# Kernel optimization log

Hardware: AMD Instinct MI355X
Metric: run time of the kernel (lower is better)

Reference implementation:

```python
import jax, jax.numpy as jnp
import numpy as np

D_MODEL = 1024
N_HEAD = 16
AGENT_NUM = 256


def setup_inputs() -> dict:
    key = jax.random.key(0)
    ks = jax.random.split(key, 11)
    B, S, D = 4, 2048, D_MODEL
    s = 1.0 / np.sqrt(D)
    return {
        "q": jax.random.normal(ks[0], (B, S, D), jnp.float32),
        "k": jax.random.normal(ks[1], (B, S, D), jnp.float32),
        "v": jax.random.normal(ks[2], (B, S, D), jnp.float32),
        "Wq": jax.random.normal(ks[3], (D, D), jnp.float32) * s,
        "bq": jnp.zeros((D,), jnp.float32),
        "Wk": jax.random.normal(ks[4], (D, D), jnp.float32) * s,
        "bk": jnp.zeros((D,), jnp.float32),
        "Wv": jax.random.normal(ks[5], (D, D), jnp.float32) * s,
        "bv": jnp.zeros((D,), jnp.float32),
        "Wo": jax.random.normal(ks[6], (D, D), jnp.float32) * s,
        "bo": jnp.zeros((D,), jnp.float32),
    }


def _split_heads(x, n_head):
    B, S, D = x.shape
    return x.reshape(B, S, n_head, D // n_head).transpose(0, 2, 1, 3)  # [B,H,S,d]


def reference(q, k, v, Wq, bq, Wk, bk, Wv, bv, Wo, bo):
    B, S, D = q.shape
    H, A = N_HEAD, AGENT_NUM
    d = D // H
    scale = 1.0 / jnp.sqrt(jnp.asarray(d, q.dtype))

    # QKV linear projections (torch Linear: x @ W.T + b)
    qh = _split_heads(q @ Wq.T + bq, H)  # [B,H,S,d]
    kh = _split_heads(k @ Wk.T + bk, H)
    vh = _split_heads(v @ Wv.T + bv, H)

    # Agent tokens: average-pool queries along sequence down to A tokens
    agent = qh.reshape(B, H, A, S // A, d).mean(axis=3)  # [B,H,A,d]

    # Stage 1: agents aggregate from keys/values (softmax over S)
    agent_attn = jax.nn.softmax(
        jnp.einsum("bhad,bhsd->bhas", agent, kh) * scale, axis=-1)  # [B,H,A,S]
    agent_v = jnp.einsum("bhas,bhsd->bhad", agent_attn, vh)  # [B,H,A,d]

    # Stage 2: queries attend to agent tokens (softmax over A)
    q_attn = jax.nn.softmax(
        jnp.einsum("bhsd,bhad->bhsa", qh, agent) * scale, axis=-1)  # [B,H,S,A]
    out_h = jnp.einsum("bhsa,bhad->bhsd", q_attn, agent_v)  # [B,H,S,d]

    # concat heads + output projection
    out = out_h.transpose(0, 2, 1, 3).reshape(B, S, D)
    out = out @ Wo.T + bo
    return out, q_attn
```

## Files before the change

kernel.cpp:

```cpp
#include <hip/hip_runtime.h>

constexpr int Bsz = 4, Ssz = 2048, Dsz = 1024, Hn = 16, dh = 64, An = 256;

typedef __attribute__((ext_vector_type(8))) short bf16x8;
typedef __attribute__((ext_vector_type(4))) float f32x4;

__device__ __forceinline__ unsigned short f2bf_rn(float f) {
    unsigned int u = __float_as_uint(f);
    return (unsigned short)((u + 0x7FFFu + ((u >> 16) & 1u)) >> 16);
}
__device__ __forceinline__ float bf2f(unsigned short h) {
    return __uint_as_float(((unsigned int)h) << 16);
}
__device__ __forceinline__ void bf_split(float f, unsigned short& hi, unsigned short& lo) {
    hi = f2bf_rn(f);
    lo = f2bf_rn(f - bf2f(hi));
}
__device__ __forceinline__ void gload16(const unsigned short* g, unsigned short* l) {
    __builtin_amdgcn_global_load_lds(
        (const __attribute__((address_space(1))) unsigned int*)g,
        (__attribute__((address_space(3))) unsigned int*)l, 16, 0, 0);
}

template<int LOGC, int NISS>
__device__ __forceinline__ void stage_tile(const unsigned short* __restrict__ g, long rowStride,
                                           unsigned short* lbase, int t) {
    const int wid = t >> 6;
    #pragma unroll
    for (int i = 0; i < NISS; ++i) {
        int slot = i * 256 + t;
        int r = slot >> LOGC;
        int c = slot & ((1 << LOGC) - 1);
        int cs = (c ^ (r & 7)) & ((1 << LOGC) - 1);
        gload16(g + (long)r * rowStride + cs * 8, lbase + (i * 256 + wid * 64) * 8);
    }
}

template<int ROWLEN>
__device__ __forceinline__ bf16x8 fragR(const unsigned short* buf, int row, int ks, int lane) {
    int c = ks * 4 + (lane >> 4);
    int cs = (c ^ (row & 7)) & (ROWLEN / 8 - 1);
    return *reinterpret_cast<const bf16x8*>(buf + row * ROWLEN + cs * 8);
}

__global__ __launch_bounds__(256)
void split_kernel(const float* __restrict__ x, unsigned short* __restrict__ hi,
                  unsigned short* __restrict__ lo, int n4)
{
    int i = blockIdx.x * 256 + threadIdx.x;
    if (i >= n4) return;
    float4 v = reinterpret_cast<const float4*>(x)[i];
    ushort4 h, l;
    bf_split(v.x, h.x, l.x);
    bf_split(v.y, h.y, l.y);
    bf_split(v.z, h.z, l.z);
    bf_split(v.w, h.w, l.w);
    reinterpret_cast<ushort4*>(hi)[i] = h;
    reinterpret_cast<ushort4*>(lo)[i] = l;
}

#define MT 128
#define BKm 32

__device__ __forceinline__ bf16x8 lds_frag(const unsigned short* buf, int baseRow, int lane) {
    int row = baseRow + (lane & 15);
    int c = lane >> 4;
    int idx = row * 32 + ((c ^ ((row >> 1) & 3)) << 3);
    return *reinterpret_cast<const bf16x8*>(buf + idx);
}

template<int OMODE>
__global__ __launch_bounds__(256, 2)
void gemm_nt_mfma3(const unsigned short* __restrict__ Ahi, const unsigned short* __restrict__ Alo,
                   const unsigned short* __restrict__ Bhi, const unsigned short* __restrict__ Blo,
                   const float* __restrict__ bias, float* __restrict__ Cf,
                   unsigned short* __restrict__ Chi, unsigned short* __restrict__ Clo,
                   int K, int N)
{
    __shared__ unsigned short lds[4 * 4096];
    const int t = threadIdx.x;
    const int lane = t & 63, wid = t >> 6;
    const int wr = wid >> 1, wc = wid & 1;
    const int m0 = blockIdx.y * MT, n0 = blockIdx.x * MT;

    const int srow0 = t >> 2;
    const int x4 = t & 3;
    const int ldsBase0 = (wid * 64) * 8;
    const int ldsBase1 = (256 + wid * 64) * 8;

    f32x4 acc[4][4];
    #pragma unroll
    for (int i = 0; i < 4; ++i)
        #pragma unroll
        for (int j = 0; j < 4; ++j)
            acc[i][j] = f32x4{0.f, 0.f, 0.f, 0.f};

    const unsigned short* gA[2] = {Ahi, Alo};
    const unsigned short* gB[2] = {Bhi, Blo};

    for (int k0 = 0; k0 < K; k0 += BKm) {
        #pragma unroll
        for (int hb = 0; hb < 2; ++hb) {
            {
                const unsigned short* G = gA[hb];
                int r0 = srow0, r1 = srow0 + 64;
                int c0 = x4 ^ ((r0 >> 1) & 3);
                int c1 = x4 ^ ((r1 >> 1) & 3);
                gload16(G + (size_t)(m0 + r0) * K + k0 + c0 * 8, lds + hb * 4096 + ldsBase0);
                gload16(G + (size_t)(m0 + r1) * K + k0 + c1 * 8, lds + hb * 4096 + ldsBase1);
            }
            {
                const unsigned short* G = gB[hb];
                int r0 = srow0, r1 = srow0 + 64;
                int c0 = x4 ^ ((r0 >> 1) & 3);
                int c1 = x4 ^ ((r1 >> 1) & 3);
                gload16(G + (size_t)(n0 + r0) * K + k0 + c0 * 8, lds + (2 + hb) * 4096 + ldsBase0);
                gload16(G + (size_t)(n0 + r1) * K + k0 + c1 * 8, lds + (2 + hb) * 4096 + ldsBase1);
            }
        }
        __syncthreads();

        bf16x8 ah[4], al[4], bh[4], bl[4];
        #pragma unroll
        for (int mi = 0; mi < 4; ++mi) {
            ah[mi] = lds_frag(lds + 0 * 4096, wr * 64 + mi * 16, lane);
            al[mi] = lds_frag(lds + 1 * 4096, wr * 64 + mi * 16, lane);
        }
        #pragma unroll
        for (int ni = 0; ni < 4; ++ni) {
            bh[ni] = lds_frag(lds + 2 * 4096, wc * 64 + ni * 16, lane);
            bl[ni] = lds_frag(lds + 3 * 4096, wc * 64 + ni * 16, lane);
        }
        #pragma unroll
        for (int mi = 0; mi < 4; ++mi)
            #pragma unroll
            for (int ni = 0; ni < 4; ++ni) {
                acc[mi][ni] = __builtin_amdgcn_mfma_f32_16x16x32_bf16(ah[mi], bh[ni], acc[mi][ni], 0, 0, 0);
                acc[mi][ni] = __builtin_amdgcn_mfma_f32_16x16x32_bf16(ah[mi], bl[ni], acc[mi][ni], 0, 0, 0);
                acc[mi][ni] = __builtin_amdgcn_mfma_f32_16x16x32_bf16(al[mi], bh[ni], acc[mi][ni], 0, 0, 0);
            }
        __syncthreads();
    }

    #pragma unroll
    for (int mi = 0; mi < 4; ++mi) {
        #pragma unroll
        for (int ni = 0; ni < 4; ++ni) {
            const int n = n0 + wc * 64 + ni * 16 + (lane & 15);
            const float bval = bias[n];
            #pragma unroll
            for (int j = 0; j < 4; ++j) {
                const int m = m0 + wr * 64 + mi * 16 + ((lane >> 4) << 2) + j;
                float val = acc[mi][ni][j] + bval;
                if constexpr (OMODE == 0) {
                    Cf[(size_t)m * N + n] = val;
                } else {
                    const int b = m >> 11, s = m & (Ssz - 1);
                    const int h = n >> 6, c = n & (dh - 1);
                    size_t idx;
                    if constexpr (OMODE == 1)
                        idx = (((size_t)(b * Hn + h)) * Ssz + s) * dh + c;
                    else
                        idx = (((size_t)(b * Hn + h)) * dh + c) * Ssz + s;
                    unsigned short hi, lo;
                    bf_split(val, hi, lo);
                    Chi[idx] = hi; Clo[idx] = lo;
                }
            }
        }
    }
}

__global__ __launch_bounds__(256)
void pool_agent(const unsigned short* __restrict__ qh_hi, const unsigned short* __restrict__ qh_lo,
                unsigned short* __restrict__ ag_hi, unsigned short* __restrict__ ag_lo)
{
    const int idx = blockIdx.x * 256 + threadIdx.x;
    const int c = idx & (dh - 1);
    const int a = (idx >> 6) & (An - 1);
    const int bh = idx >> 14;
    const size_t base = ((size_t)bh * Ssz + a * 8) * dh + c;
    float s = 0.f;
    #pragma unroll
    for (int j = 0; j < 8; ++j)
        s += bf2f(qh_hi[base + j * dh]) + bf2f(qh_lo[base + j * dh]);
    s *= 0.125f;
    unsigned short hi, lo;
    bf_split(s, hi, lo);
    ag_hi[idx] = hi; ag_lo[idx] = lo;
}

__global__ __launch_bounds__(256, 2)
void flash1(const unsigned short* __restrict__ ag_hi, const unsigned short* __restrict__ ag_lo,
            const unsigned short* __restrict__ kh_hi, const unsigned short* __restrict__ kh_lo,
            const unsigned short* __restrict__ vt_hi_g, const unsigned short* __restrict__ vt_lo_g,
            unsigned short* __restrict__ avt_hi, unsigned short* __restrict__ avt_lo)
{
    __shared__ unsigned short lds[32768];
    unsigned short* agh = lds;
    unsigned short* agl = lds + 4096;
    unsigned short* kth = lds + 8192;
    unsigned short* ktl = lds + 12288;
    unsigned short* vth = lds + 16384;
    unsigned short* vtl = lds + 20480;
    const int t = threadIdx.x;
    const int lane = t & 63, w = t >> 6;
    unsigned short* pwh = lds + 24576 + w * 2048;
    unsigned short* pwl = pwh + 1024;

    const int bh = blockIdx.y;
    const int a0 = blockIdx.x * 64;

    stage_tile<3, 2>(ag_hi + ((size_t)bh * An + a0) * dh, dh, agh, t);
    stage_tile<3, 2>(ag_lo + ((size_t)bh * An + a0) * dh, dh, agl, t);

    f32x4 O[4];
    #pragma unroll
    for (int i = 0; i < 4; ++i) O[i] = f32x4{0.f, 0.f, 0.f, 0.f};
    float m_run = -INFINITY, l_run = 0.f;

    bf16x8 bqh[2], bql[2];
    bool haveQ = false;

    for (int s0 = 0; s0 < Ssz; s0 += 64) {
        stage_tile<3, 2>(kh_hi + ((size_t)bh * Ssz + s0) * dh, dh, kth, t);
        stage_tile<3, 2>(kh_lo + ((size_t)bh * Ssz + s0) * dh, dh, ktl, t);
        stage_tile<3, 2>(vt_hi_g + (size_t)bh * dh * Ssz + s0, Ssz, vth, t);
        stage_tile<3, 2>(vt_lo_g + (size_t)bh * dh * Ssz + s0, Ssz, vtl, t);
        __syncthreads();

        if (!haveQ) {
            #pragma unroll
            for (int ks = 0; ks < 2; ++ks) {
                bqh[ks] = fragR<64>(agh, w * 16 + (lane & 15), ks, lane);
                bql[ks] = fragR<64>(agl, w * 16 + (lane & 15), ks, lane);
            }
            haveQ = true;
        }

        f32x4 sc[4];
        #pragma unroll
        for (int si = 0; si < 4; ++si) sc[si] = f32x4{0.f, 0.f, 0.f, 0.f};
        #pragma unroll
        for (int si = 0; si < 4; ++si)
            #pragma unroll
            for (int ks = 0; ks < 2; ++ks) {
                bf16x8 ah = fragR<64>(kth, si * 16 + (lane & 15), ks, lane);
                bf16x8 al = fragR<64>(ktl, si * 16 + (lane & 15), ks, lane);
                sc[si] = __builtin_amdgcn_mfma_f32_16x16x32_bf16(ah, bqh[ks], sc[si], 0, 0, 0);
                sc[si] = __builtin_amdgcn_mfma_f32_16x16x32_bf16(ah, bql[ks], sc[si], 0, 0, 0);
                sc[si] = __builtin_amdgcn_mfma_f32_16x16x32_bf16(al, bqh[ks], sc[si], 0, 0, 0);
            }

        float tmax = -INFINITY;
        #pragma unroll
        for (int si = 0; si < 4; ++si)
            #pragma unroll
            for (int j = 0; j < 4; ++j) {
                sc[si][j] *= 0.125f;
                tmax = fmaxf(tmax, sc[si][j]);
            }
        tmax = fmaxf(tmax, __shfl_xor(tmax, 16));
        tmax = fmaxf(tmax, __shfl_xor(tmax, 32));
        float newm = fmaxf(m_run, tmax);
        float fac = __expf(m_run - newm);
        float tsum = 0.f;
        #pragma unroll
        for (int si = 0; si < 4; ++si)
            #pragma unroll
            for (int j = 0; j < 4; ++j) {
                float p = __expf(sc[si][j] - newm);
                sc[si][j] = p;
                tsum += p;
            }
        tsum += __shfl_xor(tsum, 16);
        tsum += __shfl_xor(tsum, 32);
        l_run = l_run * fac + tsum;
        m_run = newm;

        const int aloc = lane & 15;
        #pragma unroll
        for (int si = 0; si < 4; ++si) {
            ushort4 h4, l4;
            bf_split(sc[si][0], h4.x, l4.x);
            bf_split(sc[si][1], h4.y, l4.y);
            bf_split(sc[si][2], h4.z, l4.z);
            bf_split(sc[si][3], h4.w, l4.w);
            int baseS = si * 16 + ((lane >> 4) << 2);
            int addr = aloc * 64 + (baseS ^ ((aloc & 7) << 3));
            *reinterpret_cast<ushort4*>(pwh + addr) = h4;
            *reinterpret_cast<ushort4*>(pwl + addr) = l4;
        }

        float fj[4];
        #pragma unroll
        for (int j = 0; j < 4; ++j) fj[j] = __shfl(fac, ((lane >> 4) << 2) + j);
        #pragma unroll
        for (int di = 0; di < 4; ++di)
            #pragma unroll
            for (int j = 0; j < 4; ++j) O[di][j] *= fj[j];

        #pragma unroll
        for (int ks = 0; ks < 2; ++ks) {
            bf16x8 pah = fragR<64>(pwh, lane & 15, ks, lane);
            bf16x8 pal = fragR<64>(pwl, lane & 15, ks, lane);
            #pragma unroll
            for (int di = 0; di < 4; ++di) {
                bf16x8 vh = fragR<64>(vth, di * 16 + (lane & 15), ks, lane);
                bf16x8 vl = fragR<64>(vtl, di * 16 + (lane & 15), ks, lane);
                O[di] = __builtin_amdgcn_mfma_f32_16x16x32_bf16(pah, vh, O[di], 0, 0, 0);
                O[di] = __builtin_amdgcn_mfma_f32_16x16x32_bf16(pah, vl, O[di], 0, 0, 0);
                O[di] = __builtin_amdgcn_mfma_f32_16x16x32_bf16(pal, vh, O[di], 0, 0, 0);
            }
        }
        __syncthreads();
    }

    float lj[4];
    #pragma unroll
    for (int j = 0; j < 4; ++j) lj[j] = __shfl(l_run, ((lane >> 4) << 2) + j);
    #pragma unroll
    for (int di = 0; di < 4; ++di)
        #pragma unroll
        for (int j = 0; j < 4; ++j) {
            float val = O[di][j] / lj[j];
            int d = di * 16 + (lane & 15);
            int aG = a0 + w * 16 + ((lane >> 4) << 2) + j;
            size_t idx = ((size_t)bh * dh + d) * An + aG;
            unsigned short hi, lo;
            bf_split(val, hi, lo);
            avt_hi[idx] = hi; avt_lo[idx] = lo;
        }
}

__global__ __launch_bounds__(256, 1)
void flash2(const unsigned short* __restrict__ qh_hi, const unsigned short* __restrict__ qh_lo,
            const unsigned short* __restrict__ ag_hi, const unsigned short* __restrict__ ag_lo,
            const unsigned short* __restrict__ avt_hi, const unsigned short* __restrict__ avt_lo,
            float* __restrict__ q_attn,
            unsigned short* __restrict__ xo_hi, unsigned short* __restrict__ xo_lo)
{
    __shared__ unsigned short lds[65536];
    unsigned short* agh = lds;
    unsigned short* agl = lds + 16384;
    unsigned short* qhh = lds + 32768;
    unsigned short* qhl = lds + 36864;

    const int t = threadIdx.x;
    const int lane = t & 63, w = t >> 6;
    unsigned short* pwh = lds + 32768 + w * 8192;
    unsigned short* pwl = pwh + 4096;

    const int bh = blockIdx.y;
    const int s0 = blockIdx.x * 64;

    stage_tile<3, 8>(ag_hi + (size_t)bh * An * dh, dh, agh, t);
    stage_tile<3, 8>(ag_lo + (size_t)bh * An * dh, dh, agl, t);
    stage_tile<3, 2>(qh_hi + ((size_t)bh * Ssz + s0) * dh, dh, qhh, t);
    stage_tile<3, 2>(qh_lo + ((size_t)bh * Ssz + s0) * dh, dh, qhl, t);
    __syncthreads();

    bf16x8 bqh[2], bql[2];
    #pragma unroll
    for (int ks = 0; ks < 2; ++ks) {
        bqh[ks] = fragR<64>(qhh, w * 16 + (lane & 15), ks, lane);
        bql[ks] = fragR<64>(qhl, w * 16 + (lane & 15), ks, lane);
    }
    __syncthreads();

    f32x4 acc[16];
    #pragma unroll
    for (int ai = 0; ai < 16; ++ai) acc[ai] = f32x4{0.f, 0.f, 0.f, 0.f};
    #pragma unroll
    for (int ai = 0; ai < 16; ++ai)
        #pragma unroll
        for (int ks = 0; ks < 2; ++ks) {
            bf16x8 ah = fragR<64>(agh, ai * 16 + (lane & 15), ks, lane);
            bf16x8 al = fragR<64>(agl, ai * 16 + (lane & 15), ks, lane);
            acc[ai] = __builtin_amdgcn_mfma_f32_16x16x32_bf16(ah, bqh[ks], acc[ai], 0, 0, 0);
            acc[ai] = __builtin_amdgcn_mfma_f32_16x16x32_bf16(ah, bql[ks], acc[ai], 0, 0, 0);
            acc[ai] = __builtin_amdgcn_mfma_f32_16x16x32_bf16(al, bqh[ks], acc[ai], 0, 0, 0);
        }

    float mx = -INFINITY;
    #pragma unroll
    for (int ai = 0; ai < 16; ++ai)
        #pragma unroll
        for (int j = 0; j < 4; ++j) {
            acc[ai][j] *= 0.125f;
            mx = fmaxf(mx, acc[ai][j]);
        }
    mx = fmaxf(mx, __shfl_xor(mx, 16));
    mx = fmaxf(mx, __shfl_xor(mx, 32));
    float sum = 0.f;
    #pragma unroll
    for (int ai = 0; ai < 16; ++ai)
        #pragma unroll
        for (int j = 0; j < 4; ++j) {
            float p = __expf(acc[ai][j] - mx);
            acc[ai][j] = p;
            sum += p;
        }
    sum += __shfl_xor(sum, 16);
    sum += __shfl_xor(sum, 32);
    const float inv = 1.0f / sum;

    {
        const int sG = s0 + w * 16 + (lane & 15);
        float* qrow = q_attn + ((size_t)bh * Ssz + sG) * An;
        const int sl = lane & 15;
        #pragma unroll
        for (int ai = 0; ai < 16; ++ai) {
            float4 o;
            o.x = acc[ai][0] * inv; o.y = acc[ai][1] * inv;
            o.z = acc[ai][2] * inv; o.w = acc[ai][3] * inv;
            *reinterpret_cast<float4*>(qrow + ai * 16 + ((lane >> 4) << 2)) = o;
            ushort4 h4, l4;
            bf_split(o.x, h4.x, l4.x);
            bf_split(o.y, h4.y, l4.y);
            bf_split(o.z, h4.z, l4.z);
            bf_split(o.w, h4.w, l4.w);
            int baseA = ai * 16 + ((lane >> 4) << 2);
            int addr = sl * 256 + (baseA ^ ((sl & 7) << 3));
            *reinterpret_cast<ushort4*>(pwh + addr) = h4;
            *reinterpret_cast<ushort4*>(pwl + addr) = l4;
        }
    }
    __syncthreads();

    stage_tile<5, 8>(avt_hi + (size_t)bh * dh * An, An, agh, t);
    stage_tile<5, 8>(avt_lo + (size_t)bh * dh * An, An, agl, t);
    __syncthreads();

    f32x4 O[4];
    #pragma unroll
    for (int i = 0; i < 4; ++i) O[i] = f32x4{0.f, 0.f, 0.f, 0.f};
    #pragma unroll
    for (int ks = 0; ks < 8; ++ks) {
        bf16x8 pah = fragR<256>(pwh, lane & 15, ks, lane);
        bf16x8 pal = fragR<256>(pwl, lane & 15, ks, lane);
        #pragma unroll
        for (int di = 0; di < 4; ++di) {
            bf16x8 avh = fragR<256>(agh, di * 16 + (lane & 15), ks, lane);
            bf16x8 avl = fragR<256>(agl, di * 16 + (lane & 15), ks, lane);
            O[di] = __builtin_amdgcn_mfma_f32_16x16x32_bf16(pah, avh, O[di], 0, 0, 0);
            O[di] = __builtin_amdgcn_mfma_f32_16x16x32_bf16(pah, avl, O[di], 0, 0, 0);
            O[di] = __builtin_amdgcn_mfma_f32_16x16x32_bf16(pal, avh, O[di], 0, 0, 0);
        }
    }

    const int b = bh >> 4, h = bh & (Hn - 1);
    #pragma unroll
    for (int di = 0; di < 4; ++di)
        #pragma unroll
        for (int j = 0; j < 4; ++j) {
            float val = O[di][j];
            int sG = s0 + w * 16 + ((lane >> 4) << 2) + j;
            int dfull = h * dh + di * 16 + (lane & 15);
            size_t idx = ((size_t)b * Ssz + sG) * Dsz + dfull;
            unsigned short hi, lo;
            bf_split(val, hi, lo);
            xo_hi[idx] = hi; xo_lo[idx] = lo;
        }
}

extern "C" void kernel_launch(void* const* d_in, const int* in_sizes, int n_in,
                              void* d_out, int out_size, void* d_ws, size_t ws_size,
                              hipStream_t stream)
{
    const float* q  = (const float*)d_in[0];
    const float* k  = (const float*)d_in[1];
    const float* v  = (const float*)d_in[2];
    const float* Wq = (const float*)d_in[3];
    const float* bq = (const float*)d_in[4];
    const float* Wk = (const float*)d_in[5];
    const float* bk = (const float*)d_in[6];
    const float* Wv = (const float*)d_in[7];
    const float* bv = (const float*)d_in[8];
    const float* Wo = (const float*)d_in[9];
    const float* bo = (const float*)d_in[10];

    constexpr size_t BSD = (size_t)Bsz * Ssz * Dsz;
    constexpr size_t DD  = (size_t)Dsz * Dsz;
    constexpr size_t AGD = (size_t)Bsz * Hn * An * dh;

    float* out    = (float*)d_out;
    float* q_attn = out + BSD;

    unsigned short* u = (unsigned short*)d_ws;
    unsigned short* x_hi   = u;
    unsigned short* x_lo   = x_hi + BSD;
    unsigned short* qh_hi  = x_lo + BSD;
    unsigned short* qh_lo  = qh_hi + BSD;
    unsigned short* kh_hi  = qh_lo + BSD;
    unsigned short* kh_lo  = kh_hi + BSD;
    unsigned short* vt_hi  = kh_lo + BSD;
    unsigned short* vt_lo  = vt_hi + BSD;
    unsigned short* w_hi   = vt_lo + BSD;
    unsigned short* w_lo   = w_hi + DD;
    unsigned short* ag_hi  = w_lo + DD;
    unsigned short* ag_lo  = ag_hi + AGD;
    unsigned short* avt_hi = ag_lo + AGD;
    unsigned short* avt_lo = avt_hi + AGD;

    const int M = Bsz * Ssz;
    dim3 gmfma(Dsz / MT, M / MT, 1);

    split_kernel<<<BSD / 1024, 256, 0, stream>>>(q, x_hi, x_lo, BSD / 4);
    split_kernel<<<DD / 1024, 256, 0, stream>>>(Wq, w_hi, w_lo, DD / 4);
    gemm_nt_mfma3<1><<<gmfma, 256, 0, stream>>>(x_hi, x_lo, w_hi, w_lo, bq, nullptr, qh_hi, qh_lo, Dsz, Dsz);
    split_kernel<<<BSD / 1024, 256, 0, stream>>>(k, x_hi, x_lo, BSD / 4);
    split_kernel<<<DD / 1024, 256, 0, stream>>>(Wk, w_hi, w_lo, DD / 4);
    gemm_nt_mfma3<1><<<gmfma, 256, 0, stream>>>(x_hi, x_lo, w_hi, w_lo, bk, nullptr, kh_hi, kh_lo, Dsz, Dsz);
    split_kernel<<<BSD / 1024, 256, 0, stream>>>(v, x_hi, x_lo, BSD / 4);
    split_kernel<<<DD / 1024, 256, 0, stream>>>(Wv, w_hi, w_lo, DD / 4);
    gemm_nt_mfma3<2><<<gmfma, 256, 0, stream>>>(x_hi, x_lo, w_hi, w_lo, bv, nullptr, vt_hi, vt_lo, Dsz, Dsz);

    pool_agent<<<AGD / 256, 256, 0, stream>>>(qh_hi, qh_lo, ag_hi, ag_lo);

    flash1<<<dim3(An / 64, Bsz * Hn), 256, 0, stream>>>(
        ag_hi, ag_lo, kh_hi, kh_lo, vt_hi, vt_lo, avt_hi, avt_lo);

    flash2<<<dim3(Ssz / 64, Bsz * Hn), 256, 0, stream>>>(
        qh_hi, qh_lo, ag_hi, ag_lo, avt_hi, avt_lo, q_attn, x_hi, x_lo);

    split_kernel<<<DD / 1024, 256, 0, stream>>>(Wo, w_hi, w_lo, DD / 4);
    gemm_nt_mfma3<0><<<gmfma, 256, 0, stream>>>(x_hi, x_lo, w_hi, w_lo, bo, out, nullptr, nullptr, Dsz, Dsz);
}
```

Baseline: 421.0 us.

## Split flash1 over sequence across waves and load fragments directly from global

flash1 now gives each block 16 agents instead of 64, and its four waves each process a quarter of the sequence. Partial softmax state and outputs are merged through LDS at the end, flash-decoding style. This quadruples the grid for better occupancy. Both flash kernels drop LDS staging of K, V, agents and queries and read MFMA fragments straight from global memory, relying on caches for reuse. Launch bounds rise to allow more resident blocks. The trade-off is more global/L2 traffic and an extra reduction step.

```diff
diff --git a/kernel.cpp b/kernel.cpp
--- a/kernel.cpp
+++ b/kernel.cpp
@@ -21,19 +21,8 @@
         (const __attribute__((address_space(1))) unsigned int*)g,
         (__attribute__((address_space(3))) unsigned int*)l, 16, 0, 0);
 }
-
-template<int LOGC, int NISS>
-__device__ __forceinline__ void stage_tile(const unsigned short* __restrict__ g, long rowStride,
-                                           unsigned short* lbase, int t) {
-    const int wid = t >> 6;
-    #pragma unroll
-    for (int i = 0; i < NISS; ++i) {
-        int slot = i * 256 + t;
-        int r = slot >> LOGC;
-        int c = slot & ((1 << LOGC) - 1);
-        int cs = (c ^ (r & 7)) & ((1 << LOGC) - 1);
-        gload16(g + (long)r * rowStride + cs * 8, lbase + (i * 256 + wid * 64) * 8);
-    }
+__device__ __forceinline__ bf16x8 gfrag(const unsigned short* g) {
+    return *reinterpret_cast<const bf16x8*>(g);
 }
 
 template<int ROWLEN>
@@ -190,67 +179,54 @@
     ag_hi[idx] = hi; ag_lo[idx] = lo;
 }
 
-__global__ __launch_bounds__(256, 2)
+__global__ __launch_bounds__(256, 3)
 void flash1(const unsigned short* __restrict__ ag_hi, const unsigned short* __restrict__ ag_lo,
             const unsigned short* __restrict__ kh_hi, const unsigned short* __restrict__ kh_lo,
-            const unsigned short* __restrict__ vt_hi_g, const unsigned short* __restrict__ vt_lo_g,
+            const unsigned short* __restrict__ vt_hi, const unsigned short* __restrict__ vt_lo,
             unsigned short* __restrict__ avt_hi, unsigned short* __restrict__ avt_lo)
 {
-    __shared__ unsigned short lds[32768];
-    unsigned short* agh = lds;
-    unsigned short* agl = lds + 4096;
-    unsigned short* kth = lds + 8192;
-    unsigned short* ktl = lds + 12288;
-    unsigned short* vth = lds + 16384;
-    unsigned short* vtl = lds + 20480;
-    const int t = threadIdx.x;
-    const int lane = t & 63, w = t >> 6;
-    unsigned short* pwh = lds + 24576 + w * 2048;
-    unsigned short* pwl = pwh + 1024;
-
-    const int bh = blockIdx.y;
-    const int a0 = blockIdx.x * 64;
-
-    stage_tile<3, 2>(ag_hi + ((size_t)bh * An + a0) * dh, dh, agh, t);
-    stage_tile<3, 2>(ag_lo + ((size_t)bh * An + a0) * dh, dh, agl, t);
+    __shared__ unsigned short pbuf[4][2][1024];
+    __shared__ float obuf[4][16][64];
+    __shared__ float mlbuf[4][2][16];
+
+    const int t = threadIdx.x, lane = t & 63, w = t >> 6;
+    const int al15 = lane & 15, hi4 = lane >> 4;
+    const int bh = blockIdx.y, a0 = blockIdx.x * 16;
+
+    const size_t agoff = ((size_t)bh * An + a0 + al15) * dh;
+    bf16x8 bqh[2], bql[2];
+    #pragma unroll
+    for (int ks = 0; ks < 2; ++ks) {
+        bqh[ks] = gfrag(ag_hi + agoff + ks * 32 + hi4 * 8);
+        bql[ks] = gfrag(ag_lo + agoff + ks * 32 + hi4 * 8);
+    }
+
+    unsigned short* pwh = pbuf[w][0];
+    unsigned short* pwl = pbuf[w][1];
 
     f32x4 O[4];
     #pragma unroll
     for (int i = 0; i < 4; ++i) O[i] = f32x4{0.f, 0.f, 0.f, 0.f};
     float m_run = -INFINITY, l_run = 0.f;
 
-    bf16x8 bqh[2], bql[2];
-    bool haveQ = false;
-
-    for (int s0 = 0; s0 < Ssz; s0 += 64) {
-        stage_tile<3, 2>(kh_hi + ((size_t)bh * Ssz + s0) * dh, dh, kth, t);
-        stage_tile<3, 2>(kh_lo + ((size_t)bh * Ssz + s0) * dh, dh, ktl, t);
-        stage_tile<3, 2>(vt_hi_g + (size_t)bh * dh * Ssz + s0, Ssz, vth, t);
-        stage_tile<3, 2>(vt_lo_g + (size_t)bh * dh * Ssz + s0, Ssz, vtl, t);
-        __syncthreads();
-
-        if (!haveQ) {
+    for (int it = 0; it < 8; ++it) {
+        const int s0 = w * 512 + it * 64;
+
+        f32x4 sc[4];
+        #pragma unroll
+        for (int si = 0; si < 4; ++si) sc[si] = f32x4{0.f, 0.f, 0.f, 0.f};
+        #pragma unroll
+        for (int si = 0; si < 4; ++si) {
+            const size_t koff = ((size_t)bh * Ssz + s0 + si * 16 + al15) * dh;
             #pragma unroll
             for (int ks = 0; ks < 2; ++ks) {
-                bqh[ks] = fragR<64>(agh, w * 16 + (lane & 15), ks, lane);
-                bql[ks] = fragR<64>(agl, w * 16 + (lane & 15), ks, lane);
-            }
-            haveQ = true;
-        }
-
-        f32x4 sc[4];
-        #pragma unroll
-        for (int si = 0; si < 4; ++si) sc[si] = f32x4{0.f, 0.f, 0.f, 0.f};
-        #pragma unroll
-        for (int si = 0; si < 4; ++si)
-            #pragma unroll
-            for (int ks = 0; ks < 2; ++ks) {
-                bf16x8 ah = fragR<64>(kth, si * 16 + (lane & 15), ks, lane);
-                bf16x8 al = fragR<64>(ktl, si * 16 + (lane & 15), ks, lane);
+                bf16x8 ah = gfrag(kh_hi + koff + ks * 32 + hi4 * 8);
+                bf16x8 al = gfrag(kh_lo + koff + ks * 32 + hi4 * 8);
                 sc[si] = __builtin_amdgcn_mfma_f32_16x16x32_bf16(ah, bqh[ks], sc[si], 0, 0, 0);
                 sc[si] = __builtin_amdgcn_mfma_f32_16x16x32_bf16(ah, bql[ks], sc[si], 0, 0, 0);
                 sc[si] = __builtin_amdgcn_mfma_f32_16x16x32_bf16(al, bqh[ks], sc[si], 0, 0, 0);
             }
+        }
 
         float tmax = -INFINITY;
         #pragma unroll
@@ -278,7 +254,6 @@
         l_run = l_run * fac + tsum;
         m_run = newm;
 
-        const int aloc = lane & 15;
         #pragma unroll
         for (int si = 0; si < 4; ++si) {
             ushort4 h4, l4;
@@ -286,15 +261,16 @@
             bf_split(sc[si][1], h4.y, l4.y);
             bf_split(sc[si][2], h4.z, l4.z);
             bf_split(sc[si][3], h4.w, l4.w);
-            int baseS = si * 16 + ((lane >> 4) << 2);
-            int addr = aloc * 64 + (baseS ^ ((aloc & 7) << 3));
+            int baseS = si * 16 + (hi4 << 2);
+            int addr = al15 * 64 + (baseS ^ ((al15 & 7) << 3));
             *reinterpret_cast<ushort4*>(pwh + addr) = h4;
             *reinterpret_cast<ushort4*>(pwl + addr) = l4;
         }
+        __syncthreads();
 
         float fj[4];
         #pragma unroll
-        for (int j = 0; j < 4; ++j) fj[j] = __shfl(fac, ((lane >> 4) << 2) + j);
+        for (int j = 0; j < 4; ++j) fj[j] = __shfl(fac, (hi4 << 2) + j);
         #pragma unroll
         for (int di = 0; di < 4; ++di)
             #pragma unroll
@@ -302,12 +278,13 @@
 
         #pragma unroll
         for (int ks = 0; ks < 2; ++ks) {
-            bf16x8 pah = fragR<64>(pwh, lane & 15, ks, lane);
-            bf16x8 pal = fragR<64>(pwl, lane & 15, ks, lane);
+            bf16x8 pah = fragR<64>(pwh, al15, ks, lane);
+            bf16x8 pal = fragR<64>(pwl, al15, ks, lane);
             #pragma unroll
             for (int di = 0; di < 4; ++di) {
-                bf16x8 vh = fragR<64>(vth, di * 16 + (lane & 15), ks, lane);
-                bf16x8 vl = fragR<64>(vtl, di * 16 + (lane & 15), ks, lane);
+                const size_t voff = ((size_t)bh * dh + di * 16 + al15) * Ssz + s0 + ks * 32 + hi4 * 8;
+                bf16x8 vh = gfrag(vt_hi + voff);
+                bf16x8 vl = gfrag(vt_lo + voff);
                 O[di] = __builtin_amdgcn_mfma_f32_16x16x32_bf16(pah, vh, O[di], 0, 0, 0);
                 O[di] = __builtin_amdgcn_mfma_f32_16x16x32_bf16(pah, vl, O[di], 0, 0, 0);
                 O[di] = __builtin_amdgcn_mfma_f32_16x16x32_bf16(pal, vh, O[di], 0, 0, 0);
@@ -316,71 +293,80 @@
         __syncthreads();
     }
 
-    float lj[4];
-    #pragma unroll
-    for (int j = 0; j < 4; ++j) lj[j] = __shfl(l_run, ((lane >> 4) << 2) + j);
     #pragma unroll
     for (int di = 0; di < 4; ++di)
         #pragma unroll
-        for (int j = 0; j < 4; ++j) {
-            float val = O[di][j] / lj[j];
-            int d = di * 16 + (lane & 15);
-            int aG = a0 + w * 16 + ((lane >> 4) << 2) + j;
-            size_t idx = ((size_t)bh * dh + d) * An + aG;
-            unsigned short hi, lo;
-            bf_split(val, hi, lo);
-            avt_hi[idx] = hi; avt_lo[idx] = lo;
-        }
-}
-
-__global__ __launch_bounds__(256, 1)
+        for (int j = 0; j < 4; ++j)
+            obuf[w][(hi4 << 2) + j][di * 16 + al15] = O[di][j];
+    if (lane < 16) {
+        mlbuf[w][0][lane] = m_run;
+        mlbuf[w][1][lane] = l_run;
+    }
+    __syncthreads();
+
+    const int d = t >> 2;
+    const int ab = (t & 3) << 2;
+    unsigned short th[4], tl[4];
+    #pragma unroll
+    for (int i = 0; i < 4; ++i) {
+        const int a = ab + i;
+        float ms = fmaxf(fmaxf(mlbuf[0][0][a], mlbuf[1][0][a]),
+                         fmaxf(mlbuf[2][0][a], mlbuf[3][0][a]));
+        float lsum = 0.f, val = 0.f;
+        #pragma unroll
+        for (int w2 = 0; w2 < 4; ++w2) {
+            float f = __expf(mlbuf[w2][0][a] - ms);
+            lsum += f * mlbuf[w2][1][a];
+            val  += f * obuf[w2][a][d];
+        }
+        val /= lsum;
+        bf_split(val, th[i], tl[i]);
+    }
+    const size_t oidx = ((size_t)bh * dh + d) * An + a0 + ab;
+    *reinterpret_cast<ushort4*>(avt_hi + oidx) = ushort4{th[0], th[1], th[2], th[3]};
+    *reinterpret_cast<ushort4*>(avt_lo + oidx) = ushort4{tl[0], tl[1], tl[2], tl[3]};
+}
+
+__global__ __launch_bounds__(256, 2)
 void flash2(const unsigned short* __restrict__ qh_hi, const unsigned short* __restrict__ qh_lo,
             const unsigned short* __restrict__ ag_hi, const unsigned short* __restrict__ ag_lo,
             const unsigned short* __restrict__ avt_hi, const unsigned short* __restrict__ avt_lo,
             float* __restrict__ q_attn,
             unsigned short* __restrict__ xo_hi, unsigned short* __restrict__ xo_lo)
 {
-    __shared__ unsigned short lds[65536];
-    unsigned short* agh = lds;
-    unsigned short* agl = lds + 16384;
-    unsigned short* qhh = lds + 32768;
-    unsigned short* qhl = lds + 36864;
-
-    const int t = threadIdx.x;
-    const int lane = t & 63, w = t >> 6;
-    unsigned short* pwh = lds + 32768 + w * 8192;
-    unsigned short* pwl = pwh + 4096;
-
+    __shared__ unsigned short pbuf[4][2][4096];
+
+    const int t = threadIdx.x, lane = t & 63, w = t >> 6;
+    const int al15 = lane & 15, hi4 = lane >> 4;
     const int bh = blockIdx.y;
     const int s0 = blockIdx.x * 64;
 
-    stage_tile<3, 8>(ag_hi + (size_t)bh * An * dh, dh, agh, t);
-    stage_tile<3, 8>(ag_lo + (size_t)bh * An * dh, dh, agl, t);
-    stage_tile<3, 2>(qh_hi + ((size_t)bh * Ssz + s0) * dh, dh, qhh, t);
-    stage_tile<3, 2>(qh_lo + ((size_t)bh * Ssz + s0) * dh, dh, qhl, t);
-    __syncthreads();
-
+    unsigned short* pwh = pbuf[w][0];
+    unsigned short* pwl = pbuf[w][1];
+
+    const size_t qoff = ((size_t)bh * Ssz + s0 + w * 16 + al15) * dh;
     bf16x8 bqh[2], bql[2];
     #pragma unroll
     for (int ks = 0; ks < 2; ++ks) {
-        bqh[ks] = fragR<64>(qhh, w * 16 + (lane & 15), ks, lane);
-        bql[ks] = fragR<64>(qhl, w * 16 + (lane & 15), ks, lane);
-    }
-    __syncthreads();
+        bqh[ks] = gfrag(qh_hi + qoff + ks * 32 + hi4 * 8);
+        bql[ks] = gfrag(qh_lo + qoff + ks * 32 + hi4 * 8);
+    }
 
     f32x4 acc[16];
     #pragma unroll
     for (int ai = 0; ai < 16; ++ai) acc[ai] = f32x4{0.f, 0.f, 0.f, 0.f};
     #pragma unroll
-    for (int ai = 0; ai < 16; ++ai)
+    for (int ai = 0; ai < 16; ++ai) {
+        const size_t aoff = ((size_t)bh * An + ai * 16 + al15) * dh;
         #pragma unroll
         for (int ks = 0; ks < 2; ++ks) {
-            bf16x8 ah = fragR<64>(agh, ai * 16 + (lane & 15), ks, lane);
-            bf16x8 al = fragR<64>(agl, ai * 16 + (lane & 15), ks, lane);
+            bf16x8 ah = gfrag(ag_hi + aoff + ks * 32 + hi4 * 8);
+            bf16x8 al = gfrag(ag_lo + aoff + ks * 32 + hi4 * 8);
             acc[ai] = __builtin_amdgcn_mfma_f32_16x16x32_bf16(ah, bqh[ks], acc[ai], 0, 0, 0);
             acc[ai] = __builtin_amdgcn_mfma_f32_16x16x32_bf16(ah, bql[ks], acc[ai], 0, 0, 0);
             acc[ai] = __builtin_amdgcn_mfma_f32_16x16x32_bf16(al, bqh[ks], acc[ai], 0, 0, 0);
         }
+    }
 
     float mx = -INFINITY;
     #pragma unroll
@@ -406,43 +392,39 @@
     const float inv = 1.0f / sum;
 
     {
-        const int sG = s0 + w * 16 + (lane & 15);
+        const int sG = s0 + w * 16 + al15;
         float* qrow = q_attn + ((size_t)bh * Ssz + sG) * An;
-        const int sl = lane & 15;
         #pragma unroll
         for (int ai = 0; ai < 16; ++ai) {
             float4 o;
             o.x = acc[ai][0] * inv; o.y = acc[ai][1] * inv;
             o.z = acc[ai][2] * inv; o.w = acc[ai][3] * inv;
-            *reinterpret_cast<float4*>(qrow + ai * 16 + ((lane >> 4) << 2)) = o;
+            *reinterpret_cast<float4*>(qrow + ai * 16 + (hi4 << 2)) = o;
             ushort4 h4, l4;
             bf_split(o.x, h4.x, l4.x);
             bf_split(o.y, h4.y, l4.y);
             bf_split(o.z, h4.z, l4.z);
             bf_split(o.w, h4.w, l4.w);
-            int baseA = ai * 16 + ((lane >> 4) << 2);
-            int addr = sl * 256 + (baseA ^ ((sl & 7) << 3));
+            int baseA = ai * 16 + (hi4 << 2);
+            int addr = al15 * 256 + (baseA ^ ((al15 & 7) << 3));
             *reinterpret_cast<ushort4*>(pwh + addr) = h4;
             *reinterpret_cast<ushort4*>(pwl + addr) = l4;
         }
     }
     __syncthreads();
 
-    stage_tile<5, 8>(avt_hi + (size_t)bh * dh * An, An, agh, t);
-    stage_tile<5, 8>(avt_lo + (size_t)bh * dh * An, An, agl, t);
-    __syncthreads();
-
     f32x4 O[4];
     #pragma unroll
     for (int i = 0; i < 4; ++i) O[i] = f32x4{0.f, 0.f, 0.f, 0.f};
     #pragma unroll
     for (int ks = 0; ks < 8; ++ks) {
-        bf16x8 pah = fragR<256>(pwh, lane & 15, ks, lane);
-        bf16x8 pal = fragR<256>(pwl, lane & 15, ks, lane);
+        bf16x8 pah = fragR<256>(pwh, al15, ks, lane);
+        bf16x8 pal = fragR<256>(pwl, al15, ks, lane);
         #pragma unroll
         for (int di = 0; di < 4; ++di) {
-            bf16x8 avh = fragR<256>(agh, di * 16 + (lane & 15), ks, lane);
-            bf16x8 avl = fragR<256>(agl, di * 16 + (lane & 15), ks, lane);
+            const size_t voff = ((size_t)bh * dh + di * 16 + al15) * An + ks * 32 + hi4 * 8;
+            bf16x8 avh = gfrag(avt_hi + voff);
+            bf16x8 avl = gfrag(avt_lo + voff);
             O[di] = __builtin_amdgcn_mfma_f32_16x16x32_bf16(pah, avh, O[di], 0, 0, 0);
             O[di] = __builtin_amdgcn_mfma_f32_16x16x32_bf16(pah, avl, O[di], 0, 0, 0);
             O[di] = __builtin_amdgcn_mfma_f32_16x16x32_bf16(pal, avh, O[di], 0, 0, 0);
@@ -455,8 +437,8 @@
         #pragma unroll
         for (int j = 0; j < 4; ++j) {
             float val = O[di][j];
-            int sG = s0 + w * 16 + ((lane >> 4) << 2) + j;
-            int dfull = h * dh + di * 16 + (lane & 15);
+            int sG = s0 + w * 16 + (hi4 << 2) + j;
+            int dfull = h * dh + di * 16 + al15;
             size_t idx = ((size_t)b * Ssz + sG) * Dsz + dfull;
             unsigned short hi, lo;
             bf_split(val, hi, lo);
@@ -518,7 +500,7 @@
 
     pool_agent<<<AGD / 256, 256, 0, stream>>>(qh_hi, qh_lo, ag_hi, ag_lo);
 
-    flash1<<<dim3(An / 64, Bsz * Hn), 256, 0, stream>>>(
+    flash1<<<dim3(An / 16, Bsz * Hn), 256, 0, stream>>>(
         ag_hi, ag_lo, kh_hi, kh_lo, vt_hi, vt_lo, avt_hi, avt_lo);
 
     flash2<<<dim3(Ssz / 64, Bsz * Hn), 256, 0, stream>>>(
```

New measurement: 529.2 us. 25.7% more time.

## Halve flash2 LDS footprint by loading Q and agent_v fragments straight from global

Applied to the files above, without the earlier changes.

The flash2 kernel no longer stages the query tile and the transposed agent_v tile through LDS. Q fragments and agent_v MFMA operands are now read directly from global memory into registers, and the per-wave probability buffers reuse the space freed by the agent tile. This halves LDS use to 64KB, so two blocks can share a CU, and the launch bound rises to 2 blocks per SM. The trade-off is that each wave re-reads agent_v from global or L2 instead of sharing one LDS copy, which adds redundant memory traffic and latency inside the inner MFMA loop.

```diff
diff --git a/kernel.cpp b/kernel.cpp
--- a/kernel.cpp
+++ b/kernel.cpp
@@ -20,6 +20,9 @@
     __builtin_amdgcn_global_load_lds(
         (const __attribute__((address_space(1))) unsigned int*)g,
         (__attribute__((address_space(3))) unsigned int*)l, 16, 0, 0);
+}
+__device__ __forceinline__ bf16x8 gfrag(const unsigned short* g) {
+    return *reinterpret_cast<const bf16x8*>(g);
 }
 
 template<int LOGC, int NISS>
@@ -333,41 +336,37 @@
         }
 }
 
-__global__ __launch_bounds__(256, 1)
+__global__ __launch_bounds__(256, 2)
 void flash2(const unsigned short* __restrict__ qh_hi, const unsigned short* __restrict__ qh_lo,
             const unsigned short* __restrict__ ag_hi, const unsigned short* __restrict__ ag_lo,
             const unsigned short* __restrict__ avt_hi, const unsigned short* __restrict__ avt_lo,
             float* __restrict__ q_attn,
             unsigned short* __restrict__ xo_hi, unsigned short* __restrict__ xo_lo)
 {
-    __shared__ unsigned short lds[65536];
+    __shared__ unsigned short lds[32768];
     unsigned short* agh = lds;
     unsigned short* agl = lds + 16384;
-    unsigned short* qhh = lds + 32768;
-    unsigned short* qhl = lds + 36864;
-
-    const int t = threadIdx.x;
-    const int lane = t & 63, w = t >> 6;
-    unsigned short* pwh = lds + 32768 + w * 8192;
-    unsigned short* pwl = pwh + 4096;
-
+
+    const int t = threadIdx.x, lane = t & 63, w = t >> 6;
+    const int al15 = lane & 15, hi4 = lane >> 4;
     const int bh = blockIdx.y;
     const int s0 = blockIdx.x * 64;
 
+    unsigned short* pwh = lds + w * 8192;
+    unsigned short* pwl = pwh + 4096;
+
     stage_tile<3, 8>(ag_hi + (size_t)bh * An * dh, dh, agh, t);
     stage_tile<3, 8>(ag_lo + (size_t)bh * An * dh, dh, agl, t);
-    stage_tile<3, 2>(qh_hi + ((size_t)bh * Ssz + s0) * dh, dh, qhh, t);
-    stage_tile<3, 2>(qh_lo + ((size_t)bh * Ssz + s0) * dh, dh, qhl, t);
+
+    const size_t qoff = ((size_t)bh * Ssz + s0 + w * 16 + al15) * dh;
+    bf16x8 bqh[2], bql[2];
+    #pragma unroll
+    for (int ks = 0; ks < 2; ++ks) {
+        bqh[ks] = gfrag(qh_hi + qoff + ks * 32 + hi4 * 8);
+        bql[ks] = gfrag(qh_lo + qoff + ks * 32 + hi4 * 8);
+    }
     __syncthreads();
 
-    bf16x8 bqh[2], bql[2];
-    #pragma unroll
-    for (int ks = 0; ks < 2; ++ks) {
-        bqh[ks] = fragR<64>(qhh, w * 16 + (lane & 15), ks, lane);
-        bql[ks] = fragR<64>(qhl, w * 16 + (lane & 15), ks, lane);
-    }
-    __syncthreads();
-
     f32x4 acc[16];
     #pragma unroll
     for (int ai = 0; ai < 16; ++ai) acc[ai] = f32x4{0.f, 0.f, 0.f, 0.f};
@@ -375,8 +374,8 @@
     for (int ai = 0; ai < 16; ++ai)
         #pragma unroll
         for (int ks = 0; ks < 2; ++ks) {
-            bf16x8 ah = fragR<64>(agh, ai * 16 + (lane & 15), ks, lane);
-            bf16x8 al = fragR<64>(agl, ai * 16 + (lane & 15), ks, lane);
+            bf16x8 ah = fragR<64>(agh, ai * 16 + al15, ks, lane);
+            bf16x8 al = fragR<64>(agl, ai * 16 + al15, ks, lane);
             acc[ai] = __builtin_amdgcn_mfma_f32_16x16x32_bf16(ah, bqh[ks], acc[ai], 0, 0, 0);
             acc[ai] = __builtin_amdgcn_mfma_f32_16x16x32_bf16(ah, bql[ks], acc[ai], 0, 0, 0);
             acc[ai] = __builtin_amdgcn_mfma_f32_16x16x32_bf16(al, bqh[ks], acc[ai], 0, 0, 0);
@@ -405,44 +404,41 @@
     sum += __shfl_xor(sum, 32);
     const float inv = 1.0f / sum;
 
+    __syncthreads();
+
     {
-        const int sG = s0 + w * 16 + (lane & 15);
+        const int sG = s0 + w * 16 + al15;
         float* qrow = q_attn + ((size_t)bh * Ssz + sG) * An;
-        const int sl = lane & 15;
         #pragma unroll
         for (int ai = 0; ai < 16; ++ai) {
             float4 o;
             o.x = acc[ai][0] * inv; o.y = acc[ai][1] * inv;
             o.z = acc[ai][2] * inv; o.w = acc[ai][3] * inv;
-            *reinterpret_cast<float4*>(qrow + ai * 16 + ((lane >> 4) << 2)) = o;
+            *reinterpret_cast<float4*>(qrow + ai * 16 + (hi4 << 2)) = o;
             ushort4 h4, l4;
             bf_split(o.x, h4.x, l4.x);
             bf_split(o.y, h4.y, l4.y);
             bf_split(o.z, h4.z, l4.z);
             bf_split(o.w, h4.w, l4.w);
-            int baseA = ai * 16 + ((lane >> 4) << 2);
-            int addr = sl * 256 + (baseA ^ ((sl & 7) << 3));
+            int baseA = ai * 16 + (hi4 << 2);
+            int addr = al15 * 256 + (baseA ^ ((al15 & 7) << 3));
             *reinterpret_cast<ushort4*>(pwh + addr) = h4;
             *reinterpret_cast<ushort4*>(pwl + addr) = l4;
         }
     }
-    __syncthreads();
-
-    stage_tile<5, 8>(avt_hi + (size_t)bh * dh * An, An, agh, t);
-    stage_tile<5, 8>(avt_lo + (size_t)bh * dh * An, An, agl, t);
-    __syncthreads();
 
     f32x4 O[4];
     #pragma unroll
     for (int i = 0; i < 4; ++i) O[i] = f32x4{0.f, 0.f, 0.f, 0.f};
     #pragma unroll
     for (int ks = 0; ks < 8; ++ks) {
-        bf16x8 pah = fragR<256>(pwh, lane & 15, ks, lane);
-        bf16x8 pal = fragR<256>(pwl, lane & 15, ks, lane);
+        bf16x8 pah = fragR<256>(pwh, al15, ks, lane);
+        bf16x8 pal = fragR<256>(pwl, al15, ks, lane);
         #pragma unroll
         for (int di = 0; di < 4; ++di) {
-            bf16x8 avh = fragR<256>(agh, di * 16 + (lane & 15), ks, lane);
-            bf16x8 avl = fragR<256>(agl, di * 16 + (lane & 15), ks, lane);
+            const size_t voff = ((size_t)bh * dh + di * 16 + al15) * An + ks * 32 + hi4 * 8;
+            bf16x8 avh = gfrag(avt_hi + voff);
+            bf16x8 avl = gfrag(avt_lo + voff);
             O[di] = __builtin_amdgcn_mfma_f32_16x16x32_bf16(pah, avh, O[di], 0, 0, 0);
             O[di] = __builtin_amdgcn_mfma_f32_16x16x32_bf16(pah, avl, O[di], 0, 0, 0);
             O[di] = __builtin_amdgcn_mfma_f32_16x16x32_bf16(pal, avh, O[di], 0, 0, 0);
@@ -455,8 +451,8 @@
         #pragma unroll
         for (int j = 0; j < 4; ++j) {
             float val = O[di][j];
-            int sG = s0 + w * 16 + ((lane >> 4) << 2) + j;
-            int dfull = h * dh + di * 16 + (lane & 15);
+            int sG = s0 + w * 16 + (hi4 << 2) + j;
+            int dfull = h * dh + di * 16 + al15;
             size_t idx = ((size_t)b * Ssz + sG) * Dsz + dfull;
             unsigned short hi, lo;
             bf_split(val, hi, lo);
```

After: 446.7 us. 1.06x slower.
